# Kernel tuning notes

Measured on AMD Instinct MI355X. Metric: run time of the kernel, lower is better.

The kernel has to match this reference:

```python
import jax, jax.numpy as jnp
import numpy as np
from math import sqrt

N_USERS = 60000
N_ITEMS = 40000
D = 64
B = 3
LAYERS = 2
E = 600000
BATCH = 2048
N_NODES = (N_USERS + 1) + (N_ITEMS + 1)
REG_WEIGHT = 1e-3
BPR_GAMMA = 1e-10


def setup_inputs() -> dict:
    key = jax.random.key(0)
    k0, k1, k2, k3, k4 = jax.random.split(key, 5)
    user_emb = jax.random.normal(k0, (N_USERS + 1, D), jnp.float32) * 0.1
    item_emb = jax.random.normal(k1, (N_ITEMS + 1, D), jnp.float32) * 0.1
    W = jnp.ones((B,), jnp.float32)
    edge_users = jax.random.randint(k2, (B, E), 1, N_USERS + 1)
    edge_items = jax.random.randint(k3, (B, E), 1, N_ITEMS + 1)
    batch_data = jax.random.randint(k4, (BATCH, B, 3), 1, N_ITEMS + 1)
    return dict(user_emb=user_emb, item_emb=item_emb, W=W,
                edge_users=edge_users, edge_items=edge_items,
                batch_data=batch_data)


def _lightgcn(emb, eu, ei, layers):
    # bipartite undirected graph: users <-> items (items offset by N_USERS+1)
    it = ei + (N_USERS + 1)
    src = jnp.concatenate([eu, it])
    dst = jnp.concatenate([it, eu])
    deg = jax.ops.segment_sum(jnp.ones_like(src, jnp.float32), src, N_NODES)
    norm = jax.lax.rsqrt(jnp.maximum(deg[src], 1.0)) * jax.lax.rsqrt(jnp.maximum(deg[dst], 1.0))
    out = emb
    cur = emb
    for _ in range(layers):
        cur = jax.ops.segment_sum(cur[src] * norm[:, None], dst, N_NODES)
        out = out + cur
    return out / (layers + 1)


def _mutual_attention(f):
    # f: [N, B, D]
    S = jnp.einsum('nid,njd->nij', f, f)          # [N, B, B] pairwise scores
    last = S[:, B - 1:B, :]                        # [N, 1, B]
    proj = S[:, :B - 1, :]                         # [N, B-1, B]
    # (last * proj) * last / (last^2 + eps)   (dim-1 is size 1, sums/norms trivial)
    clear = (last * proj) * last / (last * last + 1e-12)   # [N, B-1, B]
    scores = jnp.sum(clear, axis=1, keepdims=True) + last   # [N, 1, B]
    all_scores = jnp.concatenate([clear, scores], axis=1)   # [N, B, B]
    att = jax.nn.softmax(all_scores / sqrt(D), axis=-1)
    return jnp.einsum('nij,njd->nid', att, f)


def reference(user_emb, item_emb, W, edge_users, edge_items, batch_data):
    total0 = jnp.concatenate([user_emb, item_emb], axis=0)   # [N_NODES, D]
    # global graph = union of all behaviors
    g_eu = edge_users.reshape(-1)
    g_ei = edge_items.reshape(-1)
    all_emb = _lightgcn(total0, g_eu, g_ei, LAYERS)
    # per-behavior propagation
    u_list, i_list = [], []
    for b in range(B):
        eb = _lightgcn(all_emb, edge_users[b], edge_items[b], LAYERS)
        u_list.append(eb[:N_USERS + 1])
        i_list.append(eb[N_USERS + 1:])
    all_user = jnp.stack(u_list, axis=1)   # [n_users+1, B, D]
    all_item = jnp.stack(i_list, axis=1)   # [n_items+1, B, D]
    all_user = _mutual_attention(all_user)
    # item behaviour degree: interactions per item per behavior
    ones = jnp.ones((E,), jnp.float32)
    ibd = jnp.stack([jax.ops.segment_sum(ones, edge_items[b], N_ITEMS + 1)
                     for b in range(B)], axis=1)   # [n_items+1, B]
    weight = ibd * W
    weight = weight / (jnp.sum(weight, axis=1, keepdims=True) + 1e-8)
    item_final = jnp.sum(all_item * weight[:, :, None], axis=1)   # [n_items+1, D]
    total_loss = jnp.float32(0.0)
    for b in range(B):
        users = batch_data[:, b, 0]
        items = batch_data[:, b, 1:3]
        uf = all_user[:, b][users][:, None, :]      # [batch, 1, D]
        itf = item_final[items]                      # [batch, 2, D]
        scores = jnp.sum(uf * itf, axis=2)           # [batch, 2]
        total_loss = total_loss - jnp.mean(
            jnp.log(BPR_GAMMA + jax.nn.sigmoid(scores[:, 0] - scores[:, 1])))
    emb_loss = (jnp.linalg.norm(user_emb) + jnp.linalg.norm(item_emb)) / (N_ITEMS + 1)
    return total_loss + REG_WEIGHT * emb_loss
```

## Files before the change

### kernel.cpp

```cpp
#include <hip/hip_runtime.h>
#include <hip/hip_bf16.h>
#include <math.h>

#define NUQ 60001
#define NIQ 40001
#define NNQ 100002
#define DQ  64
#define EQ  600000
#define BQ  3
#define BATCHQ 2048
#define ROWW 32
#define NSLOT (BATCHQ * BQ)
#define NPAD 100004
#define ADJB 1200000
#define BLK_ELE 2048
#define NBLK ((NNQ + BLK_ELE - 1) / BLK_ELE)
#define RANGE 392
#define NRANGE 256
#define NBINS (BQ * NRANGE)
#define NBLKA 256
#define EPB ((BQ * EQ + NBLKA - 1) / NBLKA)

__device__ __forceinline__ float wave_sum(float v) {
#pragma unroll
  for (int m = 32; m >= 1; m >>= 1) v += __shfl_xor(v, m, 64);
  return v;
}
__device__ __forceinline__ int wave_sum_i(int v) {
#pragma unroll
  for (int m = 32; m >= 1; m >>= 1) v += __shfl_xor(v, m, 64);
  return v;
}

__device__ __forceinline__ unsigned pack_bf2(float lo, float hi) {
  unsigned a = __float_as_uint(lo);
  unsigned b = __float_as_uint(hi);
  a = (a + 0x7FFFu + ((a >> 16) & 1u)) >> 16;
  b = (b + 0x7FFFu + ((b >> 16) & 1u)) >> 16;
  return a | (b << 16);
}
__device__ __forceinline__ float unpk_lo(unsigned u) { return __uint_as_float(u << 16); }
__device__ __forceinline__ float unpk_hi(unsigned u) { return __uint_as_float(u & 0xFFFF0000u); }

__device__ __forceinline__ void ntst_u32(unsigned* p, unsigned v) { __builtin_nontemporal_store(v, p); }
__device__ __forceinline__ void ntst_f32(float* p, float v) { __builtin_nontemporal_store(v, p); }
__device__ __forceinline__ unsigned ntld_u32(const unsigned* p) { return __builtin_nontemporal_load(p); }
__device__ __forceinline__ float ntld_f32(const float* p) { return __builtin_nontemporal_load(p); }

__global__ void zero_i_k(int* __restrict__ p, int n) {
  int tid = blockIdx.x * blockDim.x + threadIdx.x;
  int stride = gridDim.x * blockDim.x;
  for (int i = tid; i < n; i += stride) p[i] = 0;
}

__global__ void sumsq_k(const float* __restrict__ p, int n, float* __restrict__ acc) {
  int tid = blockIdx.x * blockDim.x + threadIdx.x;
  int stride = gridDim.x * blockDim.x;
  float s = 0.f;
  for (int i = tid; i < n; i += stride) { float v = p[i]; s += v * v; }
  s = wave_sum(s);
  __shared__ float ws[4];
  if ((threadIdx.x & 63) == 0) ws[threadIdx.x >> 6] = s;
  __syncthreads();
  if (threadIdx.x == 0) atomicAdd(acc, ws[0] + ws[1] + ws[2] + ws[3]);
}

__global__ void binc_k(const int* __restrict__ eu, const int* __restrict__ ei,
                       unsigned* __restrict__ counts) {
  __shared__ unsigned h[NBINS];
  for (int i = threadIdx.x; i < NBINS; i += 256) h[i] = 0u;
  __syncthreads();
  int base = blockIdx.x * EPB;
  int end = base + EPB;
  if (end > BQ * EQ) end = BQ * EQ;
  for (int idx = base + threadIdx.x; idx < end; idx += 256) {
    int b = idx / EQ;
    int u = eu[idx];
    int it = ei[idx] + NUQ;
    atomicAdd(&h[b * NRANGE + u / RANGE], 1u);
    atomicAdd(&h[b * NRANGE + it / RANGE], 1u);
  }
  __syncthreads();
  for (int i = threadIdx.x; i < NBINS; i += 256)
    counts[(size_t)blockIdx.x * NBINS + i] = h[i];
}

__global__ void binscan1_k(const unsigned* __restrict__ counts,
                           unsigned* __restrict__ offs, unsigned* __restrict__ bintot) {
  int bin = blockIdx.x;
  int t = threadIdx.x;
  int lane = t & 63, wid = t >> 6;
  unsigned v = counts[(size_t)t * NBINS + bin];
  unsigned incl = v;
#pragma unroll
  for (int off = 1; off < 64; off <<= 1) {
    unsigned x = __shfl_up(incl, off, 64);
    if (lane >= off) incl += x;
  }
  __shared__ unsigned wsum[4];
  if (lane == 63) wsum[wid] = incl;
  __syncthreads();
  if (t == 0) {
    unsigned s = 0;
#pragma unroll
    for (int w = 0; w < 4; ++w) { unsigned x = wsum[w]; wsum[w] = s; s += x; }
  }
  __syncthreads();
  unsigned excl = incl - v + wsum[wid];
  offs[(size_t)t * NBINS + bin] = excl;
  if (t == 255) bintot[bin] = excl + v;
}

__global__ void binscan2_k(const unsigned* __restrict__ bintot,
                           unsigned* __restrict__ binstart) {
  int t = threadIdx.x;
  int lane = t & 63, wid = t >> 6;
  unsigned c0 = bintot[t * 3 + 0], c1 = bintot[t * 3 + 1], c2 = bintot[t * 3 + 2];
  unsigned tsum = c0 + c1 + c2;
  unsigned incl = tsum;
#pragma unroll
  for (int off = 1; off < 64; off <<= 1) {
    unsigned x = __shfl_up(incl, off, 64);
    if (lane >= off) incl += x;
  }
  __shared__ unsigned wsum[4];
  if (lane == 63) wsum[wid] = incl;
  __syncthreads();
  if (t == 0) {
    unsigned s = 0;
#pragma unroll
    for (int w = 0; w < 4; ++w) { unsigned x = wsum[w]; wsum[w] = s; s += x; }
  }
  __syncthreads();
  unsigned run = incl - tsum + wsum[wid];
  binstart[t * 3 + 0] = run; run += c0;
  binstart[t * 3 + 1] = run; run += c1;
  binstart[t * 3 + 2] = run; run += c2;
  if (t == 255) binstart[NBINS] = run;
}

__global__ void binfill_k(const int* __restrict__ eu, const int* __restrict__ ei,
                          const unsigned* __restrict__ offs,
                          const unsigned* __restrict__ binstart,
                          unsigned* __restrict__ records) {
  __shared__ unsigned cur[NBINS];
  for (int i = threadIdx.x; i < NBINS; i += 256)
    cur[i] = binstart[i] + offs[(size_t)blockIdx.x * NBINS + i];
  __syncthreads();
  int base = blockIdx.x * EPB;
  int end = base + EPB;
  if (end > BQ * EQ) end = BQ * EQ;
  for (int idx = base + threadIdx.x; idx < end; idx += 256) {
    int b = idx / EQ;
    int u = eu[idx];
    int itl = ei[idx];
    int it = itl + NUQ;
    unsigned p = atomicAdd(&cur[b * NRANGE + u / RANGE], 1u);
    records[p] = ((unsigned)(u % RANGE) << 16) | (unsigned)itl;
    unsigned q = atomicAdd(&cur[b * NRANGE + it / RANGE], 1u);
    records[q] = ((unsigned)(it % RANGE) << 16) | (unsigned)u;
  }
}

__global__ void bindeg_k(const unsigned* __restrict__ records,
                         const unsigned* __restrict__ binstart,
                         int* __restrict__ degB) {
  int bin = blockIdx.x;
  int b = bin / NRANGE;
  int r0 = (bin % NRANGE) * RANGE;
  __shared__ int h[RANGE];
  for (int i = threadIdx.x; i < RANGE; i += 256) h[i] = 0;
  __syncthreads();
  unsigned rs = binstart[bin], re = binstart[bin + 1];
  for (unsigned j = rs + threadIdx.x; j < re; j += 256)
    atomicAdd(&h[records[j] >> 16], 1);
  __syncthreads();
  int nval = NNQ - r0;
  if (nval > RANGE) nval = RANGE;
  int* deg = degB + (size_t)b * NPAD;
  for (int i = threadIdx.x; i < nval; i += 256) deg[r0 + i] = h[i];
}

__global__ void scan_p1_k(const int* __restrict__ degB, int* __restrict__ partial) {
  int b = blockIdx.x / NBLK;
  int blk = blockIdx.x % NBLK;
  const int* deg = degB + (size_t)b * NPAD;
  int base = blk * BLK_ELE + threadIdx.x * 8;
  int s = 0;
#pragma unroll
  for (int i = 0; i < 8; ++i) { int idx = base + i; if (idx < NNQ) s += deg[idx]; }
  s = wave_sum_i(s);
  __shared__ int lds[4];
  int wid = threadIdx.x >> 6;
  if ((threadIdx.x & 63) == 0) lds[wid] = s;
  __syncthreads();
  if (threadIdx.x == 0) partial[b * NBLK + blk] = lds[0] + lds[1] + lds[2] + lds[3];
}

__global__ void scan_p2_k(int* __restrict__ partial, int* __restrict__ rowptrB) {
  int wid = threadIdx.x >> 6;
  int lane = threadIdx.x & 63;
  if (wid >= BQ) return;
  int v = (lane < NBLK) ? partial[wid * NBLK + lane] : 0;
  int orig = v;
#pragma unroll
  for (int off = 1; off < 64; off <<= 1) {
    int t = __shfl_up(v, off, 64);
    if (lane >= off) v += t;
  }
  if (lane < NBLK) partial[wid * NBLK + lane] = v - orig;
  if (lane == NBLK - 1) rowptrB[(size_t)wid * NPAD + NNQ] = v;
}

__global__ void scan_p3_k(const int* __restrict__ degB, const int* __restrict__ partial,
                          int* __restrict__ rowptrB, float* __restrict__ invsqB) {
  int b = blockIdx.x / NBLK;
  int blk = blockIdx.x % NBLK;
  const int* deg = degB + (size_t)b * NPAD;
  int* rowptr = rowptrB + (size_t)b * NPAD;
  float* invsq = invsqB + (size_t)b * NPAD;
  int base = blk * BLK_ELE + threadIdx.x * 8;
  int d[8];
  int tsum = 0;
#pragma unroll
  for (int i = 0; i < 8; ++i) {
    int idx = base + i;
    d[i] = (idx < NNQ) ? deg[idx] : 0;
    tsum += d[i];
  }
  int lane = threadIdx.x & 63;
  int wid = threadIdx.x >> 6;
  int incl = tsum;
#pragma unroll
  for (int off = 1; off < 64; off <<= 1) {
    int t = __shfl_up(incl, off, 64);
    if (lane >= off) incl += t;
  }
  int excl = incl - tsum;
  __shared__ int lds[4];
  if (lane == 63) lds[wid] = incl;
  __syncthreads();
  if (threadIdx.x == 0) {
    int s = 0;
#pragma unroll
    for (int w = 0; w < 4; ++w) { int t = lds[w]; lds[w] = s; s += t; }
  }
  __syncthreads();
  int run = excl + lds[wid] + partial[b * NBLK + blk];
#pragma unroll
  for (int i = 0; i < 8; ++i) {
    int idx = base + i;
    if (idx < NNQ) {
      rowptr[idx] = run;
      run += d[i];
      invsq[idx] = rsqrtf(fmaxf((float)d[i], 1.f));
    }
  }
}

__global__ void invsqg_k(const int* __restrict__ degB, float* __restrict__ invsqG) {
  int n = blockIdx.x * blockDim.x + threadIdx.x;
  if (n >= NNQ) return;
  int dg = degB[n] + degB[NPAD + n] + degB[2 * NPAD + n];
  invsqG[n] = rsqrtf(fmaxf((float)dg, 1.f));
}

__global__ void binscat_k(const unsigned* __restrict__ records,
                          const unsigned* __restrict__ binstart,
                          const int* __restrict__ rowptrB,
                          unsigned short* __restrict__ adjB) {
  int bin = blockIdx.x;
  int b = bin / NRANGE;
  int r0 = (bin % NRANGE) * RANGE;
  int nval = NNQ - r0;
  if (nval > RANGE) nval = RANGE;
  __shared__ int cur[RANGE];
  const int* rowptr = rowptrB + (size_t)b * NPAD;
  for (int i = threadIdx.x; i < nval; i += 256) cur[i] = rowptr[r0 + i];
  __syncthreads();
  unsigned rs = binstart[bin], re = binstart[bin + 1];
  unsigned short* adj = adjB + (size_t)b * ADJB;
  for (unsigned j = rs + threadIdx.x; j < re; j += 256) {
    unsigned rec = records[j];
    int dl = rec >> 16;
    int pos = atomicAdd(&cur[dl], 1);
    adj[pos] = (unsigned short)(rec & 0xFFFFu);
  }
}

__global__ void pack_emb_k(const float* __restrict__ ue, const float* __restrict__ ie,
                           unsigned* __restrict__ E0) {
  int idx = blockIdx.x * blockDim.x + threadIdx.x;
  if (idx >= NNQ * ROWW) return;
  int n = idx >> 5, k = idx & 31;
  const float* src = (n < NUQ) ? (ue + (size_t)n * DQ) : (ie + (size_t)(n - NUQ) * DQ);
  float a = src[2 * k], b = src[2 * k + 1];
  ntst_u32(&E0[idx], pack_bf2(a, b));
}

__device__ __forceinline__ void gather_w(const unsigned* __restrict__ S,
                                         const unsigned short* __restrict__ adj,
                                         const float* __restrict__ invsq,
                                         int start, int end, int offs,
                                         int lane, unsigned k4, int g,
                                         float& alo, float& ahi) {
  for (int j0 = start; j0 < end; j0 += 64) {
    int nloc = end - j0;
    if (nloc > 64) nloc = 64;
    unsigned boff = (unsigned)offs << 7;
    float w = 0.f;
    if (lane < nloc) {
      int a = (int)adj[j0 + lane] + offs;
      boff = (unsigned)a << 7;
      w = invsq[a];
    }
    for (int j = 0; j < nloc; j += 16) {
#pragma unroll
      for (int m = 0; m < 8; ++m) {
        int jj = j + 2 * m + g;
        unsigned bo = (unsigned)__shfl((int)boff, jj, 64) + k4;
        float ww = __shfl(w, jj, 64);
        unsigned dd = *(const unsigned*)((const char*)S + bo);
        alo += ww * unpk_lo(dd);
        ahi += ww * unpk_hi(dd);
      }
    }
  }
}

__device__ __forceinline__ void gather3w(const unsigned* __restrict__ S,
                                         const unsigned short* __restrict__ adjB,
                                         const float* __restrict__ wtab,
                                         int s0, int d0, int s1, int d1,
                                         int s2, int d2, int offs,
                                         int lane, unsigned k4, int g,
                                         float& alo, float& ahi) {
  int D = d0 + d1 + d2;
  int d01 = d0 + d1;
  for (int j0 = 0; j0 < D; j0 += 64) {
    int nloc = D - j0;
    if (nloc > 64) nloc = 64;
    unsigned boff = (unsigned)offs << 7;
    float w = 0.f;
    int l = j0 + lane;
    if (l < D) {
      int idx;
      if (l < d0)       idx = s0 + l;
      else if (l < d01) idx = ADJB + s1 + (l - d0);
      else              idx = 2 * ADJB + s2 + (l - d01);
      int a = (int)adjB[idx] + offs;
      boff = (unsigned)a << 7;
      w = wtab[a];
    }
    for (int j = 0; j < nloc; j += 16) {
#pragma unroll
      for (int m = 0; m < 8; ++m) {
        int jj = j + 2 * m + g;
        unsigned bo = (unsigned)__shfl((int)boff, jj, 64) + k4;
        float ww = __shfl(w, jj, 64);
        unsigned dd = *(const unsigned*)((const char*)S + bo);
        alo += ww * unpk_lo(dd);
        ahi += ww * unpk_hi(dd);
      }
    }
  }
}

__global__ void g_l1_k(const unsigned* __restrict__ E0, unsigned* __restrict__ T1,
                       const int* __restrict__ rowptrB, const unsigned short* __restrict__ adjB,
                       const float* __restrict__ invsqG) {
  int wid = (blockIdx.x * blockDim.x + threadIdx.x) >> 6;
  int lane = threadIdx.x & 63;
  if (wid >= NNQ) return;
  int k = lane & 31, g = lane >> 5;
  unsigned k4 = (unsigned)k << 2;
  int offs = (wid < NUQ) ? NUQ : 0;
  const int* rp0 = rowptrB;
  const int* rp1 = rowptrB + NPAD;
  const int* rp2 = rowptrB + 2 * (size_t)NPAD;
  int s0 = rp0[wid], d0 = rp0[wid + 1] - s0;
  int s1 = rp1[wid], d1 = rp1[wid + 1] - s1;
  int s2 = rp2[wid], d2 = rp2[wid + 1] - s2;
  float alo = 0.f, ahi = 0.f;
  gather3w(E0, adjB, invsqG, s0, d0, s1, d1, s2, d2, offs, lane, k4, g, alo, ahi);
  alo += __shfl_xor(alo, 32, 64);
  ahi += __shfl_xor(ahi, 32, 64);
  float s = invsqG[wid];
  if (lane < 32)
    ntst_u32(&T1[(size_t)wid * ROWW + k], pack_bf2(alo * s, ahi * s));
}

__global__ void g_l2c_k(const unsigned* __restrict__ E0, const unsigned* __restrict__ T1,
                        unsigned* __restrict__ C,
                        const int* __restrict__ rowptrB, const unsigned short* __restrict__ adjB,
                        const float* __restrict__ invsqG) {
  int wid = (blockIdx.x * blockDim.x + threadIdx.x) >> 6;
  int lane = threadIdx.x & 63;
  if (wid >= NNQ) return;
  int k = lane & 31, g = lane >> 5;
  unsigned k4 = (unsigned)k << 2;
  int offs = (wid < NUQ) ? NUQ : 0;
  const int* rp0 = rowptrB;
  const int* rp1 = rowptrB + NPAD;
  const int* rp2 = rowptrB + 2 * (size_t)NPAD;
  int s0 = rp0[wid], d0 = rp0[wid + 1] - s0;
  int s1 = rp1[wid], d1 = rp1[wid + 1] - s1;
  int s2 = rp2[wid], d2 = rp2[wid + 1] - s2;
  float alo = 0.f, ahi = 0.f;
  gather3w(T1, adjB, invsqG, s0, d0, s1, d1, s2, d2, offs, lane, k4, g, alo, ahi);
  alo += __shfl_xor(alo, 32, 64);
  ahi += __shfl_xor(ahi, 32, 64);
  if (lane < 32) {
    float s = invsqG[wid];
    unsigned e0 = E0[(size_t)wid * ROWW + k];
    unsigned t1 = T1[(size_t)wid * ROWW + k];
    float clo = (unpk_lo(e0) + unpk_lo(t1) + alo * s) * (1.f / 3.f);
    float chi = (unpk_hi(e0) + unpk_hi(t1) + ahi * s) * (1.f / 3.f);
    ntst_u32(&C[(size_t)wid * ROWW + k], pack_bf2(clo, chi));
  }
}

__global__ void b_l1_k(const unsigned* __restrict__ C, unsigned* __restrict__ T1B,
                       const int* __restrict__ rowptrB, const unsigned short* __restrict__ adjB,
                       const float* __restrict__ invsqB) {
  int wid = (blockIdx.x * blockDim.x + threadIdx.x) >> 6;
  int lane = threadIdx.x & 63;
  if (wid >= NNQ) return;
  int b = blockIdx.y;
  const int* rowptr = rowptrB + (size_t)b * NPAD;
  const float* iv = invsqB + (size_t)b * NPAD;
  int k = lane & 31, g = lane >> 5;
  unsigned k4 = (unsigned)k << 2;
  int offs = (wid < NUQ) ? NUQ : 0;
  float alo = 0.f, ahi = 0.f;
  gather_w(C, adjB + (size_t)b * ADJB, iv, rowptr[wid], rowptr[wid + 1], offs, lane, k4, g, alo, ahi);
  alo += __shfl_xor(alo, 32, 64);
  ahi += __shfl_xor(ahi, 32, 64);
  float s = iv[wid];
  if (lane < 32)
    ntst_u32(&T1B[(size_t)b * NNQ * ROWW + (size_t)wid * ROWW + k], pack_bf2(alo * s, ahi * s));
}

__global__ void slot_users_k(const unsigned* __restrict__ C, const unsigned* __restrict__ T1B,
                             const int* __restrict__ rowptrB, const unsigned short* __restrict__ adjB,
                             const float* __restrict__ invsqB,
                             const int* __restrict__ batch, float* __restrict__ UG) {
  int slot = (blockIdx.x * blockDim.x + threadIdx.x) >> 6;
  int lane = threadIdx.x & 63;
  if (slot >= NSLOT) return;
  int b = blockIdx.y;
  const int* rp = rowptrB + (size_t)b * NPAD;
  const float* iv = invsqB + (size_t)b * NPAD;
  const unsigned* T1 = T1B + (size_t)b * NNQ * ROWW;
  int u = batch[slot * 3 + 0];
  int k = lane & 31, g = lane >> 5;
  unsigned k4 = (unsigned)k << 2;
  float alo = 0.f, ahi = 0.f;
  gather_w(T1, adjB + (size_t)b * ADJB, iv, rp[u], rp[u + 1], NUQ, lane, k4, g, alo, ahi);
  alo += __shfl_xor(alo, 32, 64);
  ahi += __shfl_xor(ahi, 32, 64);
  float s = iv[u];
  unsigned c0 = C[(size_t)u * ROWW + k];
  unsigned t0 = T1[(size_t)u * ROWW + k];
  if (lane < 32) {
    size_t base = ((size_t)slot * BQ + b) * DQ;
    ntst_f32(&UG[base + 2 * k],     (unpk_lo(c0) + unpk_lo(t0) + alo * s) * (1.f / 3.f));
    ntst_f32(&UG[base + 2 * k + 1], (unpk_hi(c0) + unpk_hi(t0) + ahi * s) * (1.f / 3.f));
  }
}

__global__ void slot_items_k(const unsigned* __restrict__ C, const unsigned* __restrict__ T1B,
                             const int* __restrict__ rowptrB, const unsigned short* __restrict__ adjB,
                             const float* __restrict__ invsqB,
                             const int* __restrict__ batch, float* __restrict__ IG) {
  int islot = (blockIdx.x * blockDim.x + threadIdx.x) >> 6;
  int lane = threadIdx.x & 63;
  if (islot >= 2 * NSLOT) return;
  int b = blockIdx.y;
  const int* rp = rowptrB + (size_t)b * NPAD;
  const float* iv = invsqB + (size_t)b * NPAD;
  const unsigned* T1 = T1B + (size_t)b * NNQ * ROWW;
  int slot = islot >> 1;
  int c = (islot & 1) + 1;
  int n = batch[slot * 3 + c] + NUQ;
  int k = lane & 31, g = lane >> 5;
  unsigned k4 = (unsigned)k << 2;
  float alo = 0.f, ahi = 0.f;
  gather_w(T1, adjB + (size_t)b * ADJB, iv, rp[n], rp[n + 1], 0, lane, k4, g, alo, ahi);
  alo += __shfl_xor(alo, 32, 64);
  ahi += __shfl_xor(ahi, 32, 64);
  float s = iv[n];
  unsigned c0 = C[(size_t)n * ROWW + k];
  unsigned t0 = T1[(size_t)n * ROWW + k];
  if (lane < 32) {
    size_t base = ((size_t)islot * BQ + b) * DQ;
    ntst_f32(&IG[base + 2 * k],     (unpk_lo(c0) + unpk_lo(t0) + alo * s) * (1.f / 3.f));
    ntst_f32(&IG[base + 2 * k + 1], (unpk_hi(c0) + unpk_hi(t0) + ahi * s) * (1.f / 3.f));
  }
}

__global__ void epilogue_k(const float* __restrict__ UG, const float* __restrict__ IG,
                           const int* __restrict__ degB, const int* __restrict__ batch,
                           const float* __restrict__ W, float* __restrict__ acc) {
  int slot = (blockIdx.x * blockDim.x + threadIdx.x) >> 6;
  int lane = threadIdx.x & 63;
  float val = 0.f;
  if (slot < NSLOT) {
    int bb = slot % BQ;
    size_t base = (size_t)slot * (BQ * DQ) + lane;
    float a0 = ntld_f32(&UG[base]);
    float a1 = ntld_f32(&UG[base + 64]);
    float a2 = ntld_f32(&UG[base + 128]);
    float p00 = wave_sum(a0 * a0);
    float p01 = wave_sum(a0 * a1);
    float p02 = wave_sum(a0 * a2);
    float p11 = wave_sum(a1 * a1);
    float p12 = wave_sum(a1 * a2);
    float p22 = wave_sum(a2 * a2);
    float last[3] = {p02, p12, p22};
    float S0[3] = {p00, p01, p02};
    float S1[3] = {p01, p11, p12};
    float rows[3][3];
#pragma unroll
    for (int j = 0; j < 3; ++j) {
      float l = last[j];
      float f = l * l / (l * l + 1e-12f);
      float c0 = S0[j] * f;
      float c1 = S1[j] * f;
      rows[0][j] = c0;
      rows[1][j] = c1;
      rows[2][j] = c0 + c1 + l;
    }
    float x0 = rows[bb][0] * 0.125f, x1 = rows[bb][1] * 0.125f, x2 = rows[bb][2] * 0.125f;
    float m = fmaxf(x0, fmaxf(x1, x2));
    float e0 = expf(x0 - m), e1 = expf(x1 - m), e2 = expf(x2 - m);
    float inv = 1.f / (e0 + e1 + e2);
    float uf = (e0 * a0 + e1 * a1 + e2 * a2) * inv;
    float sco[2];
#pragma unroll
    for (int c = 0; c < 2; ++c) {
      int islot = slot * 2 + c;
      int node = batch[slot * 3 + 1 + c] + NUQ;
      float w0 = (float)degB[0 * NPAD + node] * W[0];
      float w1 = (float)degB[1 * NPAD + node] * W[1];
      float w2 = (float)degB[2 * NPAD + node] * W[2];
      float inv2 = 1.f / (w0 + w1 + w2 + 1e-8f);
      size_t rb = (size_t)islot * (BQ * DQ) + lane;
      float ifv = (ntld_f32(&IG[rb]) * w0 + ntld_f32(&IG[rb + 64]) * w1 +
                   ntld_f32(&IG[rb + 128]) * w2) * inv2;
      sco[c] = wave_sum(uf * ifv);
    }
    if (lane == 0) {
      float x = sco[0] - sco[1];
      float sg = 1.f / (1.f + expf(-x));
      val = -logf(1e-10f + sg) * (1.f / (float)BATCHQ);
    }
  }
  __shared__ float ws[4];
  if (lane == 0) ws[threadIdx.x >> 6] = val;
  __syncthreads();
  if (threadIdx.x == 0) atomicAdd(acc, ws[0] + ws[1] + ws[2] + ws[3]);
}

__global__ void finalize_k(const float* __restrict__ sc, unsigned int* __restrict__ out) {
  float total = sc[0] + 0.001f * (sqrtf(sc[1]) + sqrtf(sc[2])) / (float)NIQ;
  unsigned int bits = __float_as_uint(total);
  unsigned int lsb = (bits >> 16) & 1u;
  unsigned int rb = (bits + 0x7FFFu + lsb) >> 16;
  out[0] = (rb << 16) | rb;
}

extern "C" void kernel_launch(void* const* d_in, const int* in_sizes, int n_in,
                              void* d_out, int out_size, void* d_ws, size_t ws_size,
                              hipStream_t stream) {
  const float* ue = (const float*)d_in[0];
  const float* ie = (const float*)d_in[1];
  const float* W  = (const float*)d_in[2];
  const int* eu    = (const int*)d_in[3];
  const int* ei    = (const int*)d_in[4];
  const int* batch = (const int*)d_in[5];

  unsigned* E0  = (unsigned*)d_ws;
  unsigned* T1  = E0 + (size_t)NNQ * ROWW;
  unsigned* C   = T1 + (size_t)NNQ * ROWW;
  unsigned* T1B = C + (size_t)NNQ * ROWW;
  float* UG   = (float*)(T1B + (size_t)BQ * NNQ * ROWW);
  float* IG   = UG + (size_t)NSLOT * (BQ * DQ);
  unsigned short* adjB = (unsigned short*)(IG + (size_t)2 * NSLOT * (BQ * DQ));
  int* rowptrB= (int*)(adjB + (size_t)BQ * ADJB);
  int* degB   = rowptrB + 3 * NPAD;
  float* invsqB = (float*)(degB + 3 * NPAD);
  float* invsqG = invsqB + 3 * NPAD;
  unsigned* counts = (unsigned*)(invsqG + NPAD);
  unsigned* offs   = counts + (size_t)NBLKA * NBINS;
  unsigned* bintot = offs + (size_t)NBLKA * NBINS;
  unsigned* binstart = bintot + 1024;
  unsigned* records = binstart + 1024;
  int* partial  = (int*)(records + (size_t)2 * BQ * EQ);
  float* sc   = (float*)(partial + 256);

  zero_i_k<<<1, 64, 0, stream>>>((int*)sc, 8);
  sumsq_k<<<512, 256, 0, stream>>>(ue, NUQ * DQ, sc + 1);
  sumsq_k<<<512, 256, 0, stream>>>(ie, NIQ * DQ, sc + 2);

  binc_k<<<NBLKA, 256, 0, stream>>>(eu, ei, counts);
  binscan1_k<<<NBINS, 256, 0, stream>>>(counts, offs, bintot);
  binscan2_k<<<1, 256, 0, stream>>>(bintot, binstart);
  binfill_k<<<NBLKA, 256, 0, stream>>>(eu, ei, offs, binstart, records);
  bindeg_k<<<NBINS, 256, 0, stream>>>(records, binstart, degB);
  scan_p1_k<<<BQ * NBLK, 256, 0, stream>>>(degB, partial);
  scan_p2_k<<<1, 256, 0, stream>>>(partial, rowptrB);
  scan_p3_k<<<BQ * NBLK, 256, 0, stream>>>(degB, partial, rowptrB, invsqB);
  invsqg_k<<<(NNQ + 255) / 256, 256, 0, stream>>>(degB, invsqG);
  binscat_k<<<NBINS, 256, 0, stream>>>(records, binstart, rowptrB, adjB);

  pack_emb_k<<<(NNQ * ROWW + 255) / 256, 256, 0, stream>>>(ue, ie, E0);

  const int NODE_BLKS = (NNQ + 3) / 4;

  g_l1_k<<<NODE_BLKS, 256, 0, stream>>>(E0, T1, rowptrB, adjB, invsqG);
  g_l2c_k<<<NODE_BLKS, 256, 0, stream>>>(E0, T1, C, rowptrB, adjB, invsqG);

  b_l1_k<<<dim3(NODE_BLKS, 3), 256, 0, stream>>>(C, T1B, rowptrB, adjB, invsqB);

  slot_users_k<<<dim3((NSLOT + 3) / 4, 3), 256, 0, stream>>>(C, T1B, rowptrB, adjB, invsqB, batch, UG);
  slot_items_k<<<dim3((2 * NSLOT + 3) / 4, 3), 256, 0, stream>>>(C, T1B, rowptrB, adjB, invsqB, batch, IG);
  epilogue_k<<<(NSLOT + 3) / 4, 256, 0, stream>>>(UG, IG, degB, batch, W, sc);
  finalize_k<<<1, 1, 0, stream>>>(sc, (unsigned int*)d_out);
}
```

Measured before the change: 452.1 us.

## Restructure SpMM gathers with padded 8-aligned adjacency and vectorized 16-byte row loads

Builds padded adjacency layouts: per-behavior (offset,weight) pairs padded to multiples of 8, plus a merged global adjacency with sentinel padding. Gather kernels now have each lane handle one of 8 neighbor rows and load 16 bytes of the embedding row, followed by a shuffle reduction across rows. The old shuffle-broadcast and 4-byte loads are dropped. This cuts shuffle overhead and load instruction count, but adds preprocessing kernels, extra workspace and extra memory traffic for the 8-byte adjacency entries.

```diff
diff --git a/kernel.cpp b/kernel.cpp
--- a/kernel.cpp
+++ b/kernel.cpp
@@ -13,6 +13,8 @@
 #define NSLOT (BATCHQ * BQ)
 #define NPAD 100004
 #define ADJB 1200000
+#define AOWB 1900032
+#define AOWG 4300032
 #define BLK_ELE 2048
 #define NBLK ((NNQ + BLK_ELE - 1) / BLK_ELE)
 #define RANGE 392
@@ -21,6 +23,10 @@
 #define NBLKA 256
 #define EPB ((BQ * EQ + NBLKA - 1) / NBLKA)
 
+typedef unsigned u32x4 __attribute__((ext_vector_type(4)));
+typedef unsigned u32x2 __attribute__((ext_vector_type(2)));
+typedef float    f32x4 __attribute__((ext_vector_type(4)));
+
 __device__ __forceinline__ float wave_sum(float v) {
 #pragma unroll
   for (int m = 32; m >= 1; m >>= 1) v += __shfl_xor(v, m, 64);
@@ -43,8 +49,6 @@
 __device__ __forceinline__ float unpk_hi(unsigned u) { return __uint_as_float(u & 0xFFFF0000u); }
 
 __device__ __forceinline__ void ntst_u32(unsigned* p, unsigned v) { __builtin_nontemporal_store(v, p); }
-__device__ __forceinline__ void ntst_f32(float* p, float v) { __builtin_nontemporal_store(v, p); }
-__device__ __forceinline__ unsigned ntld_u32(const unsigned* p) { return __builtin_nontemporal_load(p); }
 __device__ __forceinline__ float ntld_f32(const float* p) { return __builtin_nontemporal_load(p); }
 
 __global__ void zero_i_k(int* __restrict__ p, int n) {
@@ -268,7 +272,9 @@
 __global__ void binscat_k(const unsigned* __restrict__ records,
                           const unsigned* __restrict__ binstart,
                           const int* __restrict__ rowptrB,
-                          unsigned short* __restrict__ adjB) {
+                          const float* __restrict__ invsqB,
+                          unsigned short* __restrict__ adjB,
+                          u32x2* __restrict__ adjowB) {
   int bin = blockIdx.x;
   int b = bin / NRANGE;
   int r0 = (bin % NRANGE) * RANGE;
@@ -280,11 +286,54 @@
   __syncthreads();
   unsigned rs = binstart[bin], re = binstart[bin + 1];
   unsigned short* adj = adjB + (size_t)b * ADJB;
+  u32x2* ow = adjowB + (size_t)b * AOWB;
+  const float* iv = invsqB + (size_t)b * NPAD;
   for (unsigned j = rs + threadIdx.x; j < re; j += 256) {
     unsigned rec = records[j];
     int dl = rec >> 16;
+    unsigned nbr = rec & 0xFFFFu;
     int pos = atomicAdd(&cur[dl], 1);
-    adj[pos] = (unsigned short)(rec & 0xFFFFu);
+    adj[pos] = (unsigned short)nbr;
+    int row = r0 + dl;
+    int a2 = (int)nbr + ((row < NUQ) ? NUQ : 0);
+    u32x2 e;
+    e.x = (unsigned)a2 << 7;
+    e.y = __float_as_uint(iv[a2]);
+    ow[pos + 7 * row] = e;
+  }
+}
+
+__global__ void pad_b_k(const int* __restrict__ rowptrB, u32x2* __restrict__ adjowB) {
+  int n = blockIdx.x * blockDim.x + threadIdx.x;
+  if (n >= NNQ) return;
+  int b = blockIdx.y;
+  const int* rp = rowptrB + (size_t)b * NPAD;
+  int rs = rp[n], d = rp[n + 1] - rs;
+  int prs = rs + 7 * n;
+  int pe = prs + ((d + 7) & ~7);
+  u32x2* ow = adjowB + (size_t)b * AOWB;
+  u32x2 z = {0u, 0u};
+  for (int j = prs + d; j < pe; ++j) ow[j] = z;
+}
+
+__global__ void expand_g_k(const unsigned short* __restrict__ adjB,
+                           const int* __restrict__ rowptrB,
+                           unsigned short* __restrict__ adjG) {
+  int wid = (blockIdx.x * blockDim.x + threadIdx.x) >> 6;
+  int lane = threadIdx.x & 63;
+  if (wid >= NNQ) return;
+  int s0 = rowptrB[wid], d0 = rowptrB[wid + 1] - s0;
+  int s1 = rowptrB[NPAD + wid], d1 = rowptrB[NPAD + wid + 1] - s1;
+  int s2 = rowptrB[2 * NPAD + wid], d2 = rowptrB[2 * NPAD + wid + 1] - s2;
+  int D = d0 + d1 + d2, d01 = d0 + d1;
+  int prs = s0 + s1 + s2 + 7 * wid;
+  int pcnt = (D + 7) & ~7;
+  for (int j = lane; j < pcnt; j += 64) {
+    unsigned v = 0xFFFFu;
+    if (j < d0) v = adjB[s0 + j];
+    else if (j < d01) v = adjB[(size_t)ADJB + s1 + (j - d0)];
+    else if (j < D) v = adjB[2 * (size_t)ADJB + s2 + (j - d01)];
+    adjG[prs + j] = (unsigned short)v;
   }
 }
 
@@ -298,204 +347,253 @@
   ntst_u32(&E0[idx], pack_bf2(a, b));
 }
 
-__device__ __forceinline__ void gather_w(const unsigned* __restrict__ S,
-                                         const unsigned short* __restrict__ adj,
-                                         const float* __restrict__ invsq,
-                                         int start, int end, int offs,
-                                         int lane, unsigned k4, int g,
-                                         float& alo, float& ahi) {
-  for (int j0 = start; j0 < end; j0 += 64) {
-    int nloc = end - j0;
-    if (nloc > 64) nloc = 64;
-    unsigned boff = (unsigned)offs << 7;
-    float w = 0.f;
-    if (lane < nloc) {
-      int a = (int)adj[j0 + lane] + offs;
-      boff = (unsigned)a << 7;
-      w = invsq[a];
+
+__device__ __forceinline__ void acc8(const u32x4 dd, float w, float* lo, float* hi) {
+#pragma unroll
+  for (int i = 0; i < 4; ++i) {
+    lo[i] += w * unpk_lo(dd[i]);
+    hi[i] += w * unpk_hi(dd[i]);
+  }
+}
+
+__device__ __forceinline__ void gather_fb(const unsigned* __restrict__ S,
+                                          const u32x2* __restrict__ ow,
+                                          int prs, int pcnt, int rowsel, unsigned k16,
+                                          float* lo, float* hi) {
+  int nst = pcnt >> 3;
+  int j = prs + rowsel;
+  for (; nst >= 2; nst -= 2, j += 16) {
+    u32x2 e0 = ow[j];
+    u32x2 e1 = ow[j + 8];
+    u32x4 d0 = *(const u32x4*)((const char*)S + (e0.x + k16));
+    u32x4 d1 = *(const u32x4*)((const char*)S + (e1.x + k16));
+    acc8(d0, __uint_as_float(e0.y), lo, hi);
+    acc8(d1, __uint_as_float(e1.y), lo, hi);
+  }
+  if (nst) {
+    u32x2 e0 = ow[j];
+    u32x4 d0 = *(const u32x4*)((const char*)S + (e0.x + k16));
+    acc8(d0, __uint_as_float(e0.y), lo, hi);
+  }
+}
+
+__device__ __forceinline__ void gather_fg(const unsigned* __restrict__ S,
+                                          const unsigned short* __restrict__ adj,
+                                          const float* __restrict__ wtab,
+                                          int offs, int prs, int pcnt,
+                                          int rowsel, unsigned k16,
+                                          float* lo, float* hi) {
+  int nst = pcnt >> 3;
+  int j = prs + rowsel;
+  for (; nst >= 2; nst -= 2, j += 16) {
+    unsigned a0 = adj[j];
+    unsigned a1 = adj[j + 8];
+    int n0 = (a0 == 0xFFFFu) ? 0 : ((int)a0 + offs);
+    int n1 = (a1 == 0xFFFFu) ? 0 : ((int)a1 + offs);
+    float w0 = wtab[n0]; if (a0 == 0xFFFFu) w0 = 0.f;
+    float w1 = wtab[n1]; if (a1 == 0xFFFFu) w1 = 0.f;
+    u32x4 d0 = *(const u32x4*)((const char*)S + (((unsigned)n0 << 7) + k16));
+    u32x4 d1 = *(const u32x4*)((const char*)S + (((unsigned)n1 << 7) + k16));
+    acc8(d0, w0, lo, hi);
+    acc8(d1, w1, lo, hi);
+  }
+  if (nst) {
+    unsigned a0 = adj[j];
+    int n0 = (a0 == 0xFFFFu) ? 0 : ((int)a0 + offs);
+    float w0 = wtab[n0]; if (a0 == 0xFFFFu) w0 = 0.f;
+    u32x4 d0 = *(const u32x4*)((const char*)S + (((unsigned)n0 << 7) + k16));
+    acc8(d0, w0, lo, hi);
+  }
+}
+
+__device__ __forceinline__ void reduce_rows(float* lo, float* hi) {
+#pragma unroll
+  for (int i = 0; i < 4; ++i) {
+#pragma unroll
+    for (int m = 1; m <= 4; m <<= 1) {
+      lo[i] += __shfl_xor(lo[i], m, 64);
+      hi[i] += __shfl_xor(hi[i], m, 64);
     }
-    for (int j = 0; j < nloc; j += 16) {
-#pragma unroll
-      for (int m = 0; m < 8; ++m) {
-        int jj = j + 2 * m + g;
-        unsigned bo = (unsigned)__shfl((int)boff, jj, 64) + k4;
-        float ww = __shfl(w, jj, 64);
-        unsigned dd = *(const unsigned*)((const char*)S + bo);
-        alo += ww * unpk_lo(dd);
-        ahi += ww * unpk_hi(dd);
-      }
-    }
-  }
-}
-
-__device__ __forceinline__ void gather3w(const unsigned* __restrict__ S,
-                                         const unsigned short* __restrict__ adjB,
-                                         const float* __restrict__ wtab,
-                                         int s0, int d0, int s1, int d1,
-                                         int s2, int d2, int offs,
-                                         int lane, unsigned k4, int g,
-                                         float& alo, float& ahi) {
-  int D = d0 + d1 + d2;
-  int d01 = d0 + d1;
-  for (int j0 = 0; j0 < D; j0 += 64) {
-    int nloc = D - j0;
-    if (nloc > 64) nloc = 64;
-    unsigned boff = (unsigned)offs << 7;
-    float w = 0.f;
-    int l = j0 + lane;
-    if (l < D) {
-      int idx;
-      if (l < d0)       idx = s0 + l;
-      else if (l < d01) idx = ADJB + s1 + (l - d0);
-      else              idx = 2 * ADJB + s2 + (l - d01);
-      int a = (int)adjB[idx] + offs;
-      boff = (unsigned)a << 7;
-      w = wtab[a];
-    }
-    for (int j = 0; j < nloc; j += 16) {
-#pragma unroll
-      for (int m = 0; m < 8; ++m) {
-        int jj = j + 2 * m + g;
-        unsigned bo = (unsigned)__shfl((int)boff, jj, 64) + k4;
-        float ww = __shfl(w, jj, 64);
-        unsigned dd = *(const unsigned*)((const char*)S + bo);
-        alo += ww * unpk_lo(dd);
-        ahi += ww * unpk_hi(dd);
-      }
-    }
   }
 }
 
 __global__ void g_l1_k(const unsigned* __restrict__ E0, unsigned* __restrict__ T1,
-                       const int* __restrict__ rowptrB, const unsigned short* __restrict__ adjB,
+                       const int* __restrict__ rowptrB,
+                       const unsigned short* __restrict__ adjG,
                        const float* __restrict__ invsqG) {
   int wid = (blockIdx.x * blockDim.x + threadIdx.x) >> 6;
   int lane = threadIdx.x & 63;
   if (wid >= NNQ) return;
-  int k = lane & 31, g = lane >> 5;
-  unsigned k4 = (unsigned)k << 2;
+  int rowsel = lane & 7;
+  int sub = lane >> 3;
+  unsigned k16 = (unsigned)sub << 4;
   int offs = (wid < NUQ) ? NUQ : 0;
-  const int* rp0 = rowptrB;
-  const int* rp1 = rowptrB + NPAD;
-  const int* rp2 = rowptrB + 2 * (size_t)NPAD;
-  int s0 = rp0[wid], d0 = rp0[wid + 1] - s0;
-  int s1 = rp1[wid], d1 = rp1[wid + 1] - s1;
-  int s2 = rp2[wid], d2 = rp2[wid + 1] - s2;
-  float alo = 0.f, ahi = 0.f;
-  gather3w(E0, adjB, invsqG, s0, d0, s1, d1, s2, d2, offs, lane, k4, g, alo, ahi);
-  alo += __shfl_xor(alo, 32, 64);
-  ahi += __shfl_xor(ahi, 32, 64);
+  int r0 = rowptrB[wid], d0 = rowptrB[wid + 1] - r0;
+  int r1 = rowptrB[NPAD + wid], d1 = rowptrB[NPAD + wid + 1] - r1;
+  int r2 = rowptrB[2 * NPAD + wid], d2 = rowptrB[2 * NPAD + wid + 1] - r2;
+  int D = d0 + d1 + d2;
+  int prs = r0 + r1 + r2 + 7 * wid;
+  int pcnt = (D + 7) & ~7;
+  float lo[4] = {0.f, 0.f, 0.f, 0.f}, hi[4] = {0.f, 0.f, 0.f, 0.f};
+  gather_fg(E0, adjG, invsqG, offs, prs, pcnt, rowsel, k16, lo, hi);
+  reduce_rows(lo, hi);
   float s = invsqG[wid];
-  if (lane < 32)
-    ntst_u32(&T1[(size_t)wid * ROWW + k], pack_bf2(alo * s, ahi * s));
+  if (rowsel == 0) {
+    u32x4 o;
+#pragma unroll
+    for (int i = 0; i < 4; ++i) o[i] = pack_bf2(lo[i] * s, hi[i] * s);
+    __builtin_nontemporal_store(o, (u32x4*)&T1[(size_t)wid * ROWW + sub * 4]);
+  }
 }
 
 __global__ void g_l2c_k(const unsigned* __restrict__ E0, const unsigned* __restrict__ T1,
                         unsigned* __restrict__ C,
-                        const int* __restrict__ rowptrB, const unsigned short* __restrict__ adjB,
+                        const int* __restrict__ rowptrB,
+                        const unsigned short* __restrict__ adjG,
                         const float* __restrict__ invsqG) {
   int wid = (blockIdx.x * blockDim.x + threadIdx.x) >> 6;
   int lane = threadIdx.x & 63;
   if (wid >= NNQ) return;
-  int k = lane & 31, g = lane >> 5;
-  unsigned k4 = (unsigned)k << 2;
+  int rowsel = lane & 7;
+  int sub = lane >> 3;
+  unsigned k16 = (unsigned)sub << 4;
   int offs = (wid < NUQ) ? NUQ : 0;
-  const int* rp0 = rowptrB;
-  const int* rp1 = rowptrB + NPAD;
-  const int* rp2 = rowptrB + 2 * (size_t)NPAD;
-  int s0 = rp0[wid], d0 = rp0[wid + 1] - s0;
-  int s1 = rp1[wid], d1 = rp1[wid + 1] - s1;
-  int s2 = rp2[wid], d2 = rp2[wid + 1] - s2;
-  float alo = 0.f, ahi = 0.f;
-  gather3w(T1, adjB, invsqG, s0, d0, s1, d1, s2, d2, offs, lane, k4, g, alo, ahi);
-  alo += __shfl_xor(alo, 32, 64);
-  ahi += __shfl_xor(ahi, 32, 64);
-  if (lane < 32) {
+  int r0 = rowptrB[wid], d0 = rowptrB[wid + 1] - r0;
+  int r1 = rowptrB[NPAD + wid], d1 = rowptrB[NPAD + wid + 1] - r1;
+  int r2 = rowptrB[2 * NPAD + wid], d2 = rowptrB[2 * NPAD + wid + 1] - r2;
+  int D = d0 + d1 + d2;
+  int prs = r0 + r1 + r2 + 7 * wid;
+  int pcnt = (D + 7) & ~7;
+  float lo[4] = {0.f, 0.f, 0.f, 0.f}, hi[4] = {0.f, 0.f, 0.f, 0.f};
+  gather_fg(T1, adjG, invsqG, offs, prs, pcnt, rowsel, k16, lo, hi);
+  reduce_rows(lo, hi);
+  if (rowsel == 0) {
     float s = invsqG[wid];
-    unsigned e0 = E0[(size_t)wid * ROWW + k];
-    unsigned t1 = T1[(size_t)wid * ROWW + k];
-    float clo = (unpk_lo(e0) + unpk_lo(t1) + alo * s) * (1.f / 3.f);
-    float chi = (unpk_hi(e0) + unpk_hi(t1) + ahi * s) * (1.f / 3.f);
-    ntst_u32(&C[(size_t)wid * ROWW + k], pack_bf2(clo, chi));
+    size_t rb = (size_t)wid * ROWW + sub * 4;
+    u32x4 e0 = *(const u32x4*)&E0[rb];
+    u32x4 t1 = *(const u32x4*)&T1[rb];
+    u32x4 o;
+#pragma unroll
+    for (int i = 0; i < 4; ++i) {
+      float clo = (unpk_lo(e0[i]) + unpk_lo(t1[i]) + lo[i] * s) * (1.f / 3.f);
+      float chi = (unpk_hi(e0[i]) + unpk_hi(t1[i]) + hi[i] * s) * (1.f / 3.f);
+      o[i] = pack_bf2(clo, chi);
+    }
+    __builtin_nontemporal_store(o, (u32x4*)&C[rb]);
   }
 }
 
 __global__ void b_l1_k(const unsigned* __restrict__ C, unsigned* __restrict__ T1B,
-                       const int* __restrict__ rowptrB, const unsigned short* __restrict__ adjB,
+                       const int* __restrict__ rowptrB,
+                       const u32x2* __restrict__ adjowB,
                        const float* __restrict__ invsqB) {
   int wid = (blockIdx.x * blockDim.x + threadIdx.x) >> 6;
   int lane = threadIdx.x & 63;
   if (wid >= NNQ) return;
   int b = blockIdx.y;
-  const int* rowptr = rowptrB + (size_t)b * NPAD;
-  const float* iv = invsqB + (size_t)b * NPAD;
-  int k = lane & 31, g = lane >> 5;
-  unsigned k4 = (unsigned)k << 2;
-  int offs = (wid < NUQ) ? NUQ : 0;
-  float alo = 0.f, ahi = 0.f;
-  gather_w(C, adjB + (size_t)b * ADJB, iv, rowptr[wid], rowptr[wid + 1], offs, lane, k4, g, alo, ahi);
-  alo += __shfl_xor(alo, 32, 64);
-  ahi += __shfl_xor(ahi, 32, 64);
-  float s = iv[wid];
-  if (lane < 32)
-    ntst_u32(&T1B[(size_t)b * NNQ * ROWW + (size_t)wid * ROWW + k], pack_bf2(alo * s, ahi * s));
+  int rowsel = lane & 7;
+  int sub = lane >> 3;
+  unsigned k16 = (unsigned)sub << 4;
+  const int* rp = rowptrB + (size_t)b * NPAD;
+  int rs = rp[wid], d = rp[wid + 1] - rs;
+  int prs = rs + 7 * wid;
+  int pcnt = (d + 7) & ~7;
+  const u32x2* ow = adjowB + (size_t)b * AOWB;
+  float lo[4] = {0.f, 0.f, 0.f, 0.f}, hi[4] = {0.f, 0.f, 0.f, 0.f};
+  gather_fb(C, ow, prs, pcnt, rowsel, k16, lo, hi);
+  reduce_rows(lo, hi);
+  float s = invsqB[(size_t)b * NPAD + wid];
+  if (rowsel == 0) {
+    u32x4 o;
+#pragma unroll
+    for (int i = 0; i < 4; ++i) o[i] = pack_bf2(lo[i] * s, hi[i] * s);
+    __builtin_nontemporal_store(o, (u32x4*)&T1B[(size_t)b * NNQ * ROWW + (size_t)wid * ROWW + sub * 4]);
+  }
 }
 
 __global__ void slot_users_k(const unsigned* __restrict__ C, const unsigned* __restrict__ T1B,
-                             const int* __restrict__ rowptrB, const unsigned short* __restrict__ adjB,
+                             const int* __restrict__ rowptrB,
+                             const u32x2* __restrict__ adjowB,
                              const float* __restrict__ invsqB,
                              const int* __restrict__ batch, float* __restrict__ UG) {
   int slot = (blockIdx.x * blockDim.x + threadIdx.x) >> 6;
   int lane = threadIdx.x & 63;
   if (slot >= NSLOT) return;
   int b = blockIdx.y;
+  int rowsel = lane & 7;
+  int sub = lane >> 3;
+  unsigned k16 = (unsigned)sub << 4;
   const int* rp = rowptrB + (size_t)b * NPAD;
-  const float* iv = invsqB + (size_t)b * NPAD;
   const unsigned* T1 = T1B + (size_t)b * NNQ * ROWW;
   int u = batch[slot * 3 + 0];
-  int k = lane & 31, g = lane >> 5;
-  unsigned k4 = (unsigned)k << 2;
-  float alo = 0.f, ahi = 0.f;
-  gather_w(T1, adjB + (size_t)b * ADJB, iv, rp[u], rp[u + 1], NUQ, lane, k4, g, alo, ahi);
-  alo += __shfl_xor(alo, 32, 64);
-  ahi += __shfl_xor(ahi, 32, 64);
-  float s = iv[u];
-  unsigned c0 = C[(size_t)u * ROWW + k];
-  unsigned t0 = T1[(size_t)u * ROWW + k];
-  if (lane < 32) {
-    size_t base = ((size_t)slot * BQ + b) * DQ;
-    ntst_f32(&UG[base + 2 * k],     (unpk_lo(c0) + unpk_lo(t0) + alo * s) * (1.f / 3.f));
-    ntst_f32(&UG[base + 2 * k + 1], (unpk_hi(c0) + unpk_hi(t0) + ahi * s) * (1.f / 3.f));
+  int rs = rp[u], d = rp[u + 1] - rs;
+  int prs = rs + 7 * u;
+  int pcnt = (d + 7) & ~7;
+  const u32x2* ow = adjowB + (size_t)b * AOWB;
+  float lo[4] = {0.f, 0.f, 0.f, 0.f}, hi[4] = {0.f, 0.f, 0.f, 0.f};
+  gather_fb(T1, ow, prs, pcnt, rowsel, k16, lo, hi);
+  reduce_rows(lo, hi);
+  float s = invsqB[(size_t)b * NPAD + u];
+  if (rowsel == 0) {
+    size_t rb = (size_t)u * ROWW + sub * 4;
+    u32x4 c0 = *(const u32x4*)&C[rb];
+    u32x4 t0 = *(const u32x4*)&T1[rb];
+    size_t base = ((size_t)slot * BQ + b) * DQ + 8 * sub;
+    f32x4 o0, o1;
+    o0.x = (unpk_lo(c0[0]) + unpk_lo(t0[0]) + lo[0] * s) * (1.f / 3.f);
+    o0.y = (unpk_hi(c0[0]) + unpk_hi(t0[0]) + hi[0] * s) * (1.f / 3.f);
+    o0.z = (unpk_lo(c0[1]) + unpk_lo(t0[1]) + lo[1] * s) * (1.f / 3.f);
+    o0.w = (unpk_hi(c0[1]) + unpk_hi(t0[1]) + hi[1] * s) * (1.f / 3.f);
+    o1.x = (unpk_lo(c0[2]) + unpk_lo(t0[2]) + lo[2] * s) * (1.f / 3.f);
+    o1.y = (unpk_hi(c0[2]) + unpk_hi(t0[2]) + hi[2] * s) * (1.f / 3.f);
+    o1.z = (unpk_lo(c0[3]) + unpk_lo(t0[3]) + lo[3] * s) * (1.f / 3.f);
+    o1.w = (unpk_hi(c0[3]) + unpk_hi(t0[3]) + hi[3] * s) * (1.f / 3.f);
+    __builtin_nontemporal_store(o0, (f32x4*)&UG[base]);
+    __builtin_nontemporal_store(o1, (f32x4*)&UG[base + 4]);
   }
 }
 
 __global__ void slot_items_k(const unsigned* __restrict__ C, const unsigned* __restrict__ T1B,
-                             const int* __restrict__ rowptrB, const unsigned short* __restrict__ adjB,
+                             const int* __restrict__ rowptrB,
+                             const u32x2* __restrict__ adjowB,
                              const float* __restrict__ invsqB,
                              const int* __restrict__ batch, float* __restrict__ IG) {
   int islot = (blockIdx.x * blockDim.x + threadIdx.x) >> 6;
   int lane = threadIdx.x & 63;
   if (islot >= 2 * NSLOT) return;
   int b = blockIdx.y;
+  int rowsel = lane & 7;
+  int sub = lane >> 3;
+  unsigned k16 = (unsigned)sub << 4;
   const int* rp = rowptrB + (size_t)b * NPAD;
-  const float* iv = invsqB + (size_t)b * NPAD;
   const unsigned* T1 = T1B + (size_t)b * NNQ * ROWW;
   int slot = islot >> 1;
   int c = (islot & 1) + 1;
   int n = batch[slot * 3 + c] + NUQ;
-  int k = lane & 31, g = lane >> 5;
-  unsigned k4 = (unsigned)k << 2;
-  float alo = 0.f, ahi = 0.f;
-  gather_w(T1, adjB + (size_t)b * ADJB, iv, rp[n], rp[n + 1], 0, lane, k4, g, alo, ahi);
-  alo += __shfl_xor(alo, 32, 64);
-  ahi += __shfl_xor(ahi, 32, 64);
-  float s = iv[n];
-  unsigned c0 = C[(size_t)n * ROWW + k];
-  unsigned t0 = T1[(size_t)n * ROWW + k];
-  if (lane < 32) {
-    size_t base = ((size_t)islot * BQ + b) * DQ;
-    ntst_f32(&IG[base + 2 * k],     (unpk_lo(c0) + unpk_lo(t0) + alo * s) * (1.f / 3.f));
-    ntst_f32(&IG[base + 2 * k + 1], (unpk_hi(c0) + unpk_hi(t0) + ahi * s) * (1.f / 3.f));
+  int rs = rp[n], d = rp[n + 1] - rs;
+  int prs = rs + 7 * n;
+  int pcnt = (d + 7) & ~7;
+  const u32x2* ow = adjowB + (size_t)b * AOWB;
+  float lo[4] = {0.f, 0.f, 0.f, 0.f}, hi[4] = {0.f, 0.f, 0.f, 0.f};
+  gather_fb(T1, ow, prs, pcnt, rowsel, k16, lo, hi);
+  reduce_rows(lo, hi);
+  float s = invsqB[(size_t)b * NPAD + n];
+  if (rowsel == 0) {
+    size_t rb = (size_t)n * ROWW + sub * 4;
+    u32x4 c0 = *(const u32x4*)&C[rb];
+    u32x4 t0 = *(const u32x4*)&T1[rb];
+    size_t base = ((size_t)islot * BQ + b) * DQ + 8 * sub;
+    f32x4 o0, o1;
+    o0.x = (unpk_lo(c0[0]) + unpk_lo(t0[0]) + lo[0] * s) * (1.f / 3.f);
+    o0.y = (unpk_hi(c0[0]) + unpk_hi(t0[0]) + hi[0] * s) * (1.f / 3.f);
+    o0.z = (unpk_lo(c0[1]) + unpk_lo(t0[1]) + lo[1] * s) * (1.f / 3.f);
+    o0.w = (unpk_hi(c0[1]) + unpk_hi(t0[1]) + hi[1] * s) * (1.f / 3.f);
+    o1.x = (unpk_lo(c0[2]) + unpk_lo(t0[2]) + lo[2] * s) * (1.f / 3.f);
+    o1.y = (unpk_hi(c0[2]) + unpk_hi(t0[2]) + hi[2] * s) * (1.f / 3.f);
+    o1.z = (unpk_lo(c0[3]) + unpk_lo(t0[3]) + lo[3] * s) * (1.f / 3.f);
+    o1.w = (unpk_hi(c0[3]) + unpk_hi(t0[3]) + hi[3] * s) * (1.f / 3.f);
+    __builtin_nontemporal_store(o0, (f32x4*)&IG[base]);
+    __builtin_nontemporal_store(o1, (f32x4*)&IG[base + 4]);
   }
 }
 
@@ -586,8 +684,10 @@
   unsigned* T1B = C + (size_t)NNQ * ROWW;
   float* UG   = (float*)(T1B + (size_t)BQ * NNQ * ROWW);
   float* IG   = UG + (size_t)NSLOT * (BQ * DQ);
-  unsigned short* adjB = (unsigned short*)(IG + (size_t)2 * NSLOT * (BQ * DQ));
-  int* rowptrB= (int*)(adjB + (size_t)BQ * ADJB);
+  u32x2* adjowB = (u32x2*)(IG + (size_t)2 * NSLOT * (BQ * DQ));
+  unsigned short* adjB = (unsigned short*)(adjowB + (size_t)BQ * AOWB);
+  unsigned short* adjG = adjB + (size_t)BQ * ADJB;
+  int* rowptrB= (int*)(adjG + (size_t)AOWG);
   int* degB   = rowptrB + 3 * NPAD;
   float* invsqB = (float*)(degB + 3 * NPAD);
   float* invsqG = invsqB + 3 * NPAD;
@@ -612,19 +712,21 @@
   scan_p2_k<<<1, 256, 0, stream>>>(partial, rowptrB);
   scan_p3_k<<<BQ * NBLK, 256, 0, stream>>>(degB, partial, rowptrB, invsqB);
   invsqg_k<<<(NNQ + 255) / 256, 256, 0, stream>>>(degB, invsqG);
-  binscat_k<<<NBINS, 256, 0, stream>>>(records, binstart, rowptrB, adjB);
+  binscat_k<<<NBINS, 256, 0, stream>>>(records, binstart, rowptrB, invsqB, adjB, adjowB);
+  pad_b_k<<<dim3((NNQ + 255) / 256, 3), 256, 0, stream>>>(rowptrB, adjowB);
+
+  const int NODE_BLKS = (NNQ + 3) / 4;
+  expand_g_k<<<NODE_BLKS, 256, 0, stream>>>(adjB, rowptrB, adjG);
 
   pack_emb_k<<<(NNQ * ROWW + 255) / 256, 256, 0, stream>>>(ue, ie, E0);
 
-  const int NODE_BLKS = (NNQ + 3) / 4;
-
-  g_l1_k<<<NODE_BLKS, 256, 0, stream>>>(E0, T1, rowptrB, adjB, invsqG);
-  g_l2c_k<<<NODE_BLKS, 256, 0, stream>>>(E0, T1, C, rowptrB, adjB, invsqG);
-
-  b_l1_k<<<dim3(NODE_BLKS, 3), 256, 0, stream>>>(C, T1B, rowptrB, adjB, invsqB);
-
-  slot_users_k<<<dim3((NSLOT + 3) / 4, 3), 256, 0, stream>>>(C, T1B, rowptrB, adjB, invsqB, batch, UG);
-  slot_items_k<<<dim3((2 * NSLOT + 3) / 4, 3), 256, 0, stream>>>(C, T1B, rowptrB, adjB, invsqB, batch, IG);
+  g_l1_k<<<NODE_BLKS, 256, 0, stream>>>(E0, T1, rowptrB, adjG, invsqG);
+  g_l2c_k<<<NODE_BLKS, 256, 0, stream>>>(E0, T1, C, rowptrB, adjG, invsqG);
+
+  b_l1_k<<<dim3(NODE_BLKS, 3), 256, 0, stream>>>(C, T1B, rowptrB, adjowB, invsqB);
+
+  slot_users_k<<<dim3((NSLOT + 3) / 4, 3), 256, 0, stream>>>(C, T1B, rowptrB, adjowB, invsqB, batch, UG);
+  slot_items_k<<<dim3((2 * NSLOT + 3) / 4, 3), 256, 0, stream>>>(C, T1B, rowptrB, adjowB, invsqB, batch, IG);
   epilogue_k<<<(NSLOT + 3) / 4, 256, 0, stream>>>(UG, IG, degB, batch, W, sc);
   finalize_k<<<1, 1, 0, stream>>>(sc, (unsigned int*)d_out);
 }
```

After: 624.4 us. 1.38x slower.
